# Performance work log

Measured on AMD Instinct MI355X. Metric: run time of the kernel, lower is better.

## Reference

```python
import jax, jax.numpy as jnp
import numpy as np

N_NODES = 100000
N_EDGES = 600000
D_IN = 128
D_OUT = 128


def setup_inputs() -> dict:
    key = jax.random.key(0)
    ks = jax.random.split(key, 8)
    stdv = 1.0 / np.sqrt(D_OUT)
    return {
        "x": jax.random.normal(ks[0], (N_NODES, D_IN), dtype=jnp.float32),
        "edge_src": jax.random.randint(ks[1], (N_EDGES,), 0, N_NODES, dtype=jnp.int32),
        "edge_dst": jax.random.randint(ks[2], (N_EDGES,), 0, N_NODES, dtype=jnp.int32),
        "edge_weight": jax.random.uniform(ks[3], (N_EDGES,), dtype=jnp.float32),
        "weight_l": jax.random.uniform(ks[4], (D_IN, D_OUT), minval=-stdv, maxval=stdv, dtype=jnp.float32),
        "bias_l": jax.random.uniform(ks[5], (D_OUT,), minval=-stdv, maxval=stdv, dtype=jnp.float32),
        "weight_r": jax.random.uniform(ks[6], (D_IN, D_OUT), minval=-stdv, maxval=stdv, dtype=jnp.float32),
        "bias_r": jax.random.uniform(ks[7], (D_OUT,), minval=-stdv, maxval=stdv, dtype=jnp.float32),
    }


def reference(x, edge_src, edge_dst, edge_weight, weight_l, bias_l, weight_r, bias_r):
    # h = input @ weight_l  -> [N, D_OUT]
    h = x @ weight_l
    # spmm(adj, h): out[dst] += adj[dst, src] * h[src]
    msgs = h[edge_src] * edge_weight[:, None]          # [E, D_OUT] gather
    agg = jax.ops.segment_sum(msgs, edge_dst, num_segments=N_NODES)
    out = agg + bias_l
    # root_weight branch (size is None)
    out = out + x @ weight_r + bias_r
    return out
```

## Files before the change

### kernel.cpp

```cpp
#include <hip/hip_runtime.h>
#include <hip/hip_bf16.h>

#define D 128
#define SCAN_BLK 256
#define SCAN_VPT 4
#define SCAN_TILE (SCAN_BLK * SCAN_VPT)

typedef __attribute__((ext_vector_type(8))) short short8;
typedef __attribute__((ext_vector_type(4))) float f32x4;

__global__ __launch_bounds__(256) void prep_w(
    const float* __restrict__ Wl, const float* __restrict__ Wr,
    const float* __restrict__ bl, const float* __restrict__ br,
    __hip_bfloat16* __restrict__ WTl, __hip_bfloat16* __restrict__ WTr,
    float* __restrict__ bsum) {
  const int tid = blockIdx.x * 256 + threadIdx.x;
  const int n = (tid >> 7) & 127;
  const int k = tid & 127;
  if (tid < 16384) {
    WTl[n * D + k] = __float2bfloat16(Wl[k * D + n]);
  } else {
    WTr[n * D + k] = __float2bfloat16(Wr[k * D + n]);
  }
  if (tid < 128) bsum[tid] = bl[tid] + br[tid];
}

__global__ __launch_bounds__(256) void gemm_h(
    const float* __restrict__ x, const __hip_bfloat16* __restrict__ WTl,
    __hip_bfloat16* __restrict__ h,
    const int* __restrict__ edst, int* __restrict__ deg, int n_edges,
    int n_rowtiles) {
  const int gsz = gridDim.x * 256;
  for (int e = blockIdx.x * 256 + threadIdx.x; e < n_edges; e += gsz)
    atomicAdd(&deg[edst[e]], 1);

  __shared__ __hip_bfloat16 xs[16][136];
  const int t = threadIdx.x;
  const int wave = t >> 6;
  const int lane = t & 63;
  const int m = lane & 15;
  const int q = lane >> 4;

  short8 bfrag[2][4];
#pragma unroll
  for (int c = 0; c < 2; ++c) {
    const int n0 = wave * 32 + c * 16;
#pragma unroll
    for (int ks = 0; ks < 4; ++ks)
      bfrag[c][ks] = *(const short8*)&WTl[(n0 + m) * D + ks * 32 + q * 8];
  }

  const int srow = t >> 4;
  const int scol = (t & 15) * 8;

  for (int rt = blockIdx.x; rt < n_rowtiles; rt += gridDim.x) {
    const int rowbase = rt * 16;
    {
      const float4* src = (const float4*)&x[(size_t)(rowbase + srow) * D + scol];
      const float4 v0 = src[0], v1 = src[1];
      __hip_bfloat16* dst = &xs[srow][scol];
      dst[0] = __float2bfloat16(v0.x); dst[1] = __float2bfloat16(v0.y);
      dst[2] = __float2bfloat16(v0.z); dst[3] = __float2bfloat16(v0.w);
      dst[4] = __float2bfloat16(v1.x); dst[5] = __float2bfloat16(v1.y);
      dst[6] = __float2bfloat16(v1.z); dst[7] = __float2bfloat16(v1.w);
    }
    __syncthreads();

    f32x4 acc[2];
#pragma unroll
    for (int c = 0; c < 2; ++c)
#pragma unroll
      for (int r = 0; r < 4; ++r) acc[c][r] = 0.f;

#pragma unroll
    for (int ks = 0; ks < 4; ++ks) {
      const short8 afrag = *(const short8*)&xs[m][ks * 32 + q * 8];
#pragma unroll
      for (int c = 0; c < 2; ++c)
        acc[c] = __builtin_amdgcn_mfma_f32_16x16x32_bf16(afrag, bfrag[c][ks], acc[c], 0, 0, 0);
    }

#pragma unroll
    for (int c = 0; c < 2; ++c) {
      const int n = wave * 32 + c * 16 + m;
#pragma unroll
      for (int r = 0; r < 4; ++r)
        h[(size_t)(rowbase + q * 4 + r) * D + n] = __float2bfloat16(acc[c][r]);
    }
    __syncthreads();
  }
}

__global__ __launch_bounds__(SCAN_BLK) void scan1_kernel(
    const int* __restrict__ deg, int* __restrict__ offsets,
    int* __restrict__ partials, int n) {
  __shared__ int sdata[SCAN_BLK];
  const int t = threadIdx.x;
  const int base = blockIdx.x * SCAN_TILE + t * SCAN_VPT;

  int v[SCAN_VPT];
  int s = 0;
#pragma unroll
  for (int j = 0; j < SCAN_VPT; ++j) {
    v[j] = (base + j < n) ? deg[base + j] : 0;
    s += v[j];
  }
  sdata[t] = s;
  __syncthreads();
  for (int off = 1; off < SCAN_BLK; off <<= 1) {
    int xv = (t >= off) ? sdata[t - off] : 0;
    __syncthreads();
    sdata[t] += xv;
    __syncthreads();
  }
  int excl = sdata[t] - s;
  if (t == SCAN_BLK - 1) partials[blockIdx.x] = sdata[t];
  int run = excl;
#pragma unroll
  for (int j = 0; j < SCAN_VPT; ++j) {
    if (base + j < n) offsets[base + j] = run;
    run += v[j];
  }
}

__global__ __launch_bounds__(SCAN_BLK) void scan3_kernel(
    int* __restrict__ offsets, int* __restrict__ pos,
    const int* __restrict__ partials, int n, int n_edges) {
  __shared__ int s_add;
  const int t = threadIdx.x;
  if (t < 64) {
    int v = 0;
    for (int j = t; j < blockIdx.x; j += 64) v += partials[j];
#pragma unroll
    for (int off = 32; off > 0; off >>= 1) v += __shfl_down(v, off);
    if (t == 0) s_add = v;
  }
  __syncthreads();
  const int add = s_add;
  const int base = blockIdx.x * SCAN_TILE + t * SCAN_VPT;
#pragma unroll
  for (int j = 0; j < SCAN_VPT; ++j) {
    const int i = base + j;
    if (i < n) {
      const int o = offsets[i] + add;
      offsets[i] = o;
      pos[i] = o;
    }
  }
  if (blockIdx.x == 0 && t == 0) offsets[n] = n_edges;
}

__global__ __launch_bounds__(256) void scatter_kernel(
    const int* __restrict__ esrc, const int* __restrict__ edst,
    const float* __restrict__ ew, int* __restrict__ pos,
    int2* __restrict__ pairs, int n_edges) {
  const int e = blockIdx.x * 256 + threadIdx.x;
  if (e >= n_edges) return;
  const int d = edst[e];
  const int slot = atomicAdd(&pos[d], 1);
  pairs[slot] = make_int2(esrc[e], __float_as_int(ew[e]));
}

__global__ __launch_bounds__(256) void sage_out(
    const float* __restrict__ x, const __hip_bfloat16* __restrict__ WTr,
    const float* __restrict__ bsum, const __hip_bfloat16* __restrict__ h,
    const int* __restrict__ offsets, const int2* __restrict__ pairs,
    float* __restrict__ out) {
  __shared__ __hip_bfloat16 xs[16][136];
  __shared__ float ot[16][D];
  const int t = threadIdx.x;
  const int wave = t >> 6;
  const int lane = t & 63;
  const int m = lane & 15;
  const int q = lane >> 4;
  const int rowbase = blockIdx.x * 16;

  short8 bfrag[2][4];
#pragma unroll
  for (int c = 0; c < 2; ++c) {
    const int n0 = wave * 32 + c * 16;
#pragma unroll
    for (int ks = 0; ks < 4; ++ks)
      bfrag[c][ks] = *(const short8*)&WTr[(n0 + m) * D + ks * 32 + q * 8];
  }

  {
    const int srow = t >> 4;
    const int scol = (t & 15) * 8;
    const float4* src = (const float4*)&x[(size_t)(rowbase + srow) * D + scol];
    const float4 v0 = src[0], v1 = src[1];
    __hip_bfloat16* dst = &xs[srow][scol];
    dst[0] = __float2bfloat16(v0.x); dst[1] = __float2bfloat16(v0.y);
    dst[2] = __float2bfloat16(v0.z); dst[3] = __float2bfloat16(v0.w);
    dst[4] = __float2bfloat16(v1.x); dst[5] = __float2bfloat16(v1.y);
    dst[6] = __float2bfloat16(v1.z); dst[7] = __float2bfloat16(v1.w);
  }
  __syncthreads();

  f32x4 acc[2];
#pragma unroll
  for (int c = 0; c < 2; ++c)
#pragma unroll
    for (int r = 0; r < 4; ++r) acc[c][r] = 0.f;

#pragma unroll
  for (int ks = 0; ks < 4; ++ks) {
    const short8 afrag = *(const short8*)&xs[m][ks * 32 + q * 8];
#pragma unroll
    for (int c = 0; c < 2; ++c)
      acc[c] = __builtin_amdgcn_mfma_f32_16x16x32_bf16(afrag, bfrag[c][ks], acc[c], 0, 0, 0);
  }

#pragma unroll
  for (int c = 0; c < 2; ++c) {
    const int n = wave * 32 + c * 16 + m;
    const float b = bsum[n];
#pragma unroll
    for (int r = 0; r < 4; ++r)
      ot[q * 4 + r][n] = acc[c][r] + b;
  }
  __syncthreads();

  const __hip_bfloat162* __restrict__ h2 = (const __hip_bfloat162*)h;
#pragma unroll
  for (int j = 0; j < 4; ++j) {
    const int ln = wave * 4 + j;
    const int node = rowbase + ln;
    const int begin = offsets[node];
    const int end = offsets[node + 1];

    float2 a = *(const float2*)&ot[ln][2 * lane];

    int i = begin;
    for (; i + 4 <= end; i += 4) {
      const int2 p0 = pairs[i + 0];
      const int2 p1 = pairs[i + 1];
      const int2 p2 = pairs[i + 2];
      const int2 p3 = pairs[i + 3];
      const __hip_bfloat162 a0 = h2[(size_t)p0.x * (D / 2) + lane];
      const __hip_bfloat162 a1 = h2[(size_t)p1.x * (D / 2) + lane];
      const __hip_bfloat162 a2 = h2[(size_t)p2.x * (D / 2) + lane];
      const __hip_bfloat162 a3 = h2[(size_t)p3.x * (D / 2) + lane];
      const float w0 = __int_as_float(p0.y), w1 = __int_as_float(p1.y);
      const float w2 = __int_as_float(p2.y), w3 = __int_as_float(p3.y);
      a.x = fmaf(w0, __bfloat162float(a0.x), a.x);
      a.y = fmaf(w0, __bfloat162float(a0.y), a.y);
      a.x = fmaf(w1, __bfloat162float(a1.x), a.x);
      a.y = fmaf(w1, __bfloat162float(a1.y), a.y);
      a.x = fmaf(w2, __bfloat162float(a2.x), a.x);
      a.y = fmaf(w2, __bfloat162float(a2.y), a.y);
      a.x = fmaf(w3, __bfloat162float(a3.x), a.x);
      a.y = fmaf(w3, __bfloat162float(a3.y), a.y);
    }
    for (; i < end; ++i) {
      const int2 p = pairs[i];
      const __hip_bfloat162 av = h2[(size_t)p.x * (D / 2) + lane];
      const float w = __int_as_float(p.y);
      a.x = fmaf(w, __bfloat162float(av.x), a.x);
      a.y = fmaf(w, __bfloat162float(av.y), a.y);
    }
    *(float2*)&out[(size_t)node * D + 2 * lane] = a;
  }
}

extern "C" void kernel_launch(void* const* d_in, const int* in_sizes, int n_in,
                              void* d_out, int out_size, void* d_ws, size_t ws_size,
                              hipStream_t stream) {
  const float* x   = (const float*)d_in[0];
  const int* esrc  = (const int*)d_in[1];
  const int* edst  = (const int*)d_in[2];
  const float* ew  = (const float*)d_in[3];
  const float* Wl  = (const float*)d_in[4];
  const float* bl  = (const float*)d_in[5];
  const float* Wr  = (const float*)d_in[6];
  const float* br  = (const float*)d_in[7];
  float* out = (float*)d_out;

  const int n_nodes = in_sizes[0] / D;
  const int n_edges = in_sizes[1];

  char* ws = (char*)d_ws;
  size_t off = 0;
  __hip_bfloat16* h = (__hip_bfloat16*)(ws + off);
  off += (size_t)n_nodes * D * sizeof(__hip_bfloat16);
  off = (off + 15) & ~15ull;
  int* offsets = (int*)(ws + off);
  off += (size_t)(n_nodes + 1) * sizeof(int);
  off = (off + 15) & ~15ull;
  int* pos = (int*)(ws + off);
  off += (size_t)n_nodes * sizeof(int);
  off = (off + 15) & ~15ull;
  int* partials = (int*)(ws + off);
  off += 1024 * sizeof(int);
  off = (off + 15) & ~15ull;
  int2* pairs = (int2*)(ws + off);
  off += (size_t)n_edges * sizeof(int2);
  off = (off + 15) & ~15ull;
  __hip_bfloat16* WTl = (__hip_bfloat16*)(ws + off);
  off += (size_t)D * D * sizeof(__hip_bfloat16);
  __hip_bfloat16* WTr = (__hip_bfloat16*)(ws + off);
  off += (size_t)D * D * sizeof(__hip_bfloat16);
  float* bsum = (float*)(ws + off);
  off += D * sizeof(float);

  const int n_rowtiles = (n_nodes + 15) / 16;

  hipMemsetAsync(pos, 0, (size_t)n_nodes * sizeof(int), stream);
  prep_w<<<128, 256, 0, stream>>>(Wl, Wr, bl, br, WTl, WTr, bsum);

  const int gemm_grid = n_rowtiles < 2048 ? n_rowtiles : 2048;
  gemm_h<<<gemm_grid, 256, 0, stream>>>(x, WTl, h, edst, pos, n_edges, n_rowtiles);

  const int nparts = (n_nodes + SCAN_TILE - 1) / SCAN_TILE;
  scan1_kernel<<<nparts, SCAN_BLK, 0, stream>>>(pos, offsets, partials, n_nodes);
  scan3_kernel<<<nparts, SCAN_BLK, 0, stream>>>(offsets, pos, partials, n_nodes, n_edges);
  scatter_kernel<<<(n_edges + 255) / 256, 256, 0, stream>>>(esrc, edst, ew, pos, pairs, n_edges);

  sage_out<<<n_rowtiles, 256, 0, stream>>>(x, WTr, bsum, h, offsets, pairs, out);
}
```

Measured before the change: 236.8 us.

## Fuse memset into prep kernel and replace two-pass scan with decoupled lookback

Folds the pos memset and scan-state reset into the weight-prep kernel, and merges the two scan kernels into a single decoupled-lookback scan that chains block prefixes through flag-tagged state words. It also overlaps the xs and ot shared buffers in sage_out, padding ot rows to 130 floats, which needs an extra barrier. The goal is fewer launches and less launch overhead. The scan reads deg from pos and writes offsets back into pos in the same kernel; each thread reads only its own entries before writing them, so this is safe, but the lookback spin relies on earlier blocks being scheduled first.

```diff
diff --git a/kernel.cpp b/kernel.cpp
--- a/kernel.cpp
+++ b/kernel.cpp
@@ -9,20 +9,22 @@
 typedef __attribute__((ext_vector_type(8))) short short8;
 typedef __attribute__((ext_vector_type(4))) float f32x4;
 
-__global__ __launch_bounds__(256) void prep_w(
+__global__ __launch_bounds__(256) void prep_zero(
     const float* __restrict__ Wl, const float* __restrict__ Wr,
     const float* __restrict__ bl, const float* __restrict__ br,
     __hip_bfloat16* __restrict__ WTl, __hip_bfloat16* __restrict__ WTr,
-    float* __restrict__ bsum) {
-  const int tid = blockIdx.x * 256 + threadIdx.x;
-  const int n = (tid >> 7) & 127;
-  const int k = tid & 127;
-  if (tid < 16384) {
+    float* __restrict__ bsum, int* __restrict__ pos,
+    unsigned long long* __restrict__ scan_state, int n_nodes) {
+  const int gtid = blockIdx.x * 256 + threadIdx.x;
+  const int gsz = gridDim.x * 256;
+  for (int i = gtid; i < D * D; i += gsz) {
+    const int n = i >> 7, k = i & 127;
     WTl[n * D + k] = __float2bfloat16(Wl[k * D + n]);
-  } else {
     WTr[n * D + k] = __float2bfloat16(Wr[k * D + n]);
   }
-  if (tid < 128) bsum[tid] = bl[tid] + br[tid];
+  if (gtid < D) bsum[gtid] = bl[gtid] + br[gtid];
+  for (int i = gtid; i < n_nodes; i += gsz) pos[i] = 0;
+  if (gtid < 128) scan_state[gtid] = 0ull;
 }
 
 __global__ __launch_bounds__(256) void gemm_h(
@@ -65,13 +67,11 @@
       dst[6] = __float2bfloat16(v1.z); dst[7] = __float2bfloat16(v1.w);
     }
     __syncthreads();
-
     f32x4 acc[2];
 #pragma unroll
     for (int c = 0; c < 2; ++c)
 #pragma unroll
       for (int r = 0; r < 4; ++r) acc[c][r] = 0.f;
-
 #pragma unroll
     for (int ks = 0; ks < 4; ++ks) {
       const short8 afrag = *(const short8*)&xs[m][ks * 32 + q * 8];
@@ -79,7 +79,6 @@
       for (int c = 0; c < 2; ++c)
         acc[c] = __builtin_amdgcn_mfma_f32_16x16x32_bf16(afrag, bfrag[c][ks], acc[c], 0, 0, 0);
     }
-
 #pragma unroll
     for (int c = 0; c < 2; ++c) {
       const int n = wave * 32 + c * 16 + m;
@@ -91,12 +90,15 @@
   }
 }
 
-__global__ __launch_bounds__(SCAN_BLK) void scan1_kernel(
+__global__ __launch_bounds__(SCAN_BLK) void scan_lb(
     const int* __restrict__ deg, int* __restrict__ offsets,
-    int* __restrict__ partials, int n) {
+    int* __restrict__ pos, unsigned long long* __restrict__ state,
+    int n, int n_edges) {
   __shared__ int sdata[SCAN_BLK];
+  __shared__ int s_base;
   const int t = threadIdx.x;
-  const int base = blockIdx.x * SCAN_TILE + t * SCAN_VPT;
+  const int b = blockIdx.x;
+  const int base = b * SCAN_TILE + t * SCAN_VPT;
 
   int v[SCAN_VPT];
   int s = 0;
@@ -113,41 +115,46 @@
     sdata[t] += xv;
     __syncthreads();
   }
-  int excl = sdata[t] - s;
-  if (t == SCAN_BLK - 1) partials[blockIdx.x] = sdata[t];
-  int run = excl;
-#pragma unroll
-  for (int j = 0; j < SCAN_VPT; ++j) {
-    if (base + j < n) offsets[base + j] = run;
-    run += v[j];
-  }
-}
-
-__global__ __launch_bounds__(SCAN_BLK) void scan3_kernel(
-    int* __restrict__ offsets, int* __restrict__ pos,
-    const int* __restrict__ partials, int n, int n_edges) {
-  __shared__ int s_add;
-  const int t = threadIdx.x;
-  if (t < 64) {
-    int v = 0;
-    for (int j = t; j < blockIdx.x; j += 64) v += partials[j];
-#pragma unroll
-    for (int off = 32; off > 0; off >>= 1) v += __shfl_down(v, off);
-    if (t == 0) s_add = v;
-  }
-  __syncthreads();
-  const int add = s_add;
-  const int base = blockIdx.x * SCAN_TILE + t * SCAN_VPT;
+  const int excl = sdata[t] - s;
+  const int total = sdata[SCAN_BLK - 1];
+
+  if (t == 0) {
+    if (b == 0) {
+      __hip_atomic_store(&state[0], (2ull << 32) | (unsigned)total,
+                         __ATOMIC_RELEASE, __HIP_MEMORY_SCOPE_AGENT);
+      s_base = 0;
+    } else {
+      __hip_atomic_store(&state[b], (1ull << 32) | (unsigned)total,
+                         __ATOMIC_RELEASE, __HIP_MEMORY_SCOPE_AGENT);
+      int run = 0;
+      int j = b - 1;
+      while (true) {
+        const unsigned long long st = __hip_atomic_load(
+            &state[j], __ATOMIC_ACQUIRE, __HIP_MEMORY_SCOPE_AGENT);
+        const unsigned flag = (unsigned)(st >> 32);
+        if (flag == 0) { __builtin_amdgcn_s_sleep(1); continue; }
+        run += (int)(unsigned)st;
+        if (flag == 2) break;
+        --j;
+      }
+      __hip_atomic_store(&state[b], (2ull << 32) | (unsigned)(run + total),
+                         __ATOMIC_RELEASE, __HIP_MEMORY_SCOPE_AGENT);
+      s_base = run;
+    }
+  }
+  __syncthreads();
+
+  int run2 = s_base + excl;
 #pragma unroll
   for (int j = 0; j < SCAN_VPT; ++j) {
     const int i = base + j;
     if (i < n) {
-      const int o = offsets[i] + add;
-      offsets[i] = o;
-      pos[i] = o;
-    }
-  }
-  if (blockIdx.x == 0 && t == 0) offsets[n] = n_edges;
+      offsets[i] = run2;
+      pos[i] = run2;
+      run2 += v[j];
+    }
+  }
+  if (b == 0 && t == 0) offsets[n] = n_edges;
 }
 
 __global__ __launch_bounds__(256) void scatter_kernel(
@@ -166,8 +173,10 @@
     const float* __restrict__ bsum, const __hip_bfloat16* __restrict__ h,
     const int* __restrict__ offsets, const int2* __restrict__ pairs,
     float* __restrict__ out) {
-  __shared__ __hip_bfloat16 xs[16][136];
-  __shared__ float ot[16][D];
+  __shared__ __align__(16) char smraw[16 * 130 * 4];
+  __hip_bfloat16 (*xs)[136] = (__hip_bfloat16(*)[136])smraw;
+  float (*ot)[130] = (float(*)[130])smraw;
+
   const int t = threadIdx.x;
   const int wave = t >> 6;
   const int lane = t & 63;
@@ -202,7 +211,6 @@
   for (int c = 0; c < 2; ++c)
 #pragma unroll
     for (int r = 0; r < 4; ++r) acc[c][r] = 0.f;
-
 #pragma unroll
   for (int ks = 0; ks < 4; ++ks) {
     const short8 afrag = *(const short8*)&xs[m][ks * 32 + q * 8];
@@ -210,6 +218,7 @@
     for (int c = 0; c < 2; ++c)
       acc[c] = __builtin_amdgcn_mfma_f32_16x16x32_bf16(afrag, bfrag[c][ks], acc[c], 0, 0, 0);
   }
+  __syncthreads();
 
 #pragma unroll
   for (int c = 0; c < 2; ++c) {
@@ -228,9 +237,7 @@
     const int node = rowbase + ln;
     const int begin = offsets[node];
     const int end = offsets[node + 1];
-
     float2 a = *(const float2*)&ot[ln][2 * lane];
-
     int i = begin;
     for (; i + 4 <= end; i += 4) {
       const int2 p0 = pairs[i + 0];
@@ -290,9 +297,8 @@
   int* pos = (int*)(ws + off);
   off += (size_t)n_nodes * sizeof(int);
   off = (off + 15) & ~15ull;
-  int* partials = (int*)(ws + off);
-  off += 1024 * sizeof(int);
-  off = (off + 15) & ~15ull;
+  unsigned long long* scan_state = (unsigned long long*)(ws + off);
+  off += 128 * sizeof(unsigned long long);
   int2* pairs = (int2*)(ws + off);
   off += (size_t)n_edges * sizeof(int2);
   off = (off + 15) & ~15ull;
@@ -305,15 +311,16 @@
 
   const int n_rowtiles = (n_nodes + 15) / 16;
 
-  hipMemsetAsync(pos, 0, (size_t)n_nodes * sizeof(int), stream);
-  prep_w<<<128, 256, 0, stream>>>(Wl, Wr, bl, br, WTl, WTr, bsum);
+  prep_zero<<<256, 256, 0, stream>>>(Wl, Wr, bl, br, WTl, WTr, bsum, pos,
+                                     scan_state, n_nodes);
 
   const int gemm_grid = n_rowtiles < 2048 ? n_rowtiles : 2048;
   gemm_h<<<gemm_grid, 256, 0, stream>>>(x, WTl, h, edst, pos, n_edges, n_rowtiles);
 
   const int nparts = (n_nodes + SCAN_TILE - 1) / SCAN_TILE;
-  scan1_kernel<<<nparts, SCAN_BLK, 0, stream>>>(pos, offsets, partials, n_nodes);
-  scan3_kernel<<<nparts, SCAN_BLK, 0, stream>>>(offsets, pos, partials, n_nodes, n_edges);
+  scan_lb<<<nparts, SCAN_BLK, 0, stream>>>(pos, offsets, pos, scan_state,
+                                           n_nodes, n_edges);
+
   scatter_kernel<<<(n_edges + 255) / 256, 256, 0, stream>>>(esrc, edst, ew, pos, pairs, n_edges);
 
   sage_out<<<n_rowtiles, 256, 0, stream>>>(x, WTr, bsum, h, offsets, pairs, out);
```

After: 248.3 us. 1.05x slower.

## Aggregate raw features before projection and fuse both GEMMs into one kernel

Applied to the files above, without the earlier changes.

Uses associativity to reorder the SAGE layer: raw fp32 x rows are gathered and summed per destination first, and (A·x)·Wl is computed afterwards instead of A·(x·Wl). This removes the separate h GEMM kernel. Both projections now run in one MFMA kernel that reads the bf16 aggregate and x together. The edge-degree histogram moves into the weight-prep kernel. In exchange the gather reads fp32 x rows (twice the bytes of the old bf16 h), and the aggregate is rounded to bf16 before the GEMM.

```diff
diff --git a/kernel.cpp b/kernel.cpp
--- a/kernel.cpp
+++ b/kernel.cpp
@@ -9,86 +9,21 @@
 typedef __attribute__((ext_vector_type(8))) short short8;
 typedef __attribute__((ext_vector_type(4))) float f32x4;
 
-__global__ __launch_bounds__(256) void prep_w(
+__global__ __launch_bounds__(256) void prep_hist(
     const float* __restrict__ Wl, const float* __restrict__ Wr,
     const float* __restrict__ bl, const float* __restrict__ br,
     __hip_bfloat16* __restrict__ WTl, __hip_bfloat16* __restrict__ WTr,
-    float* __restrict__ bsum) {
-  const int tid = blockIdx.x * 256 + threadIdx.x;
-  const int n = (tid >> 7) & 127;
-  const int k = tid & 127;
-  if (tid < 16384) {
+    float* __restrict__ bsum, int* __restrict__ pos,
+    const int* __restrict__ edst, int n_edges) {
+  const int gtid = blockIdx.x * 256 + threadIdx.x;
+  const int gsz = gridDim.x * 256;
+  for (int i = gtid; i < D * D; i += gsz) {
+    const int k = i >> 7, n = i & 127;
     WTl[n * D + k] = __float2bfloat16(Wl[k * D + n]);
-  } else {
     WTr[n * D + k] = __float2bfloat16(Wr[k * D + n]);
   }
-  if (tid < 128) bsum[tid] = bl[tid] + br[tid];
-}
-
-__global__ __launch_bounds__(256) void gemm_h(
-    const float* __restrict__ x, const __hip_bfloat16* __restrict__ WTl,
-    __hip_bfloat16* __restrict__ h,
-    const int* __restrict__ edst, int* __restrict__ deg, int n_edges,
-    int n_rowtiles) {
-  const int gsz = gridDim.x * 256;
-  for (int e = blockIdx.x * 256 + threadIdx.x; e < n_edges; e += gsz)
-    atomicAdd(&deg[edst[e]], 1);
-
-  __shared__ __hip_bfloat16 xs[16][136];
-  const int t = threadIdx.x;
-  const int wave = t >> 6;
-  const int lane = t & 63;
-  const int m = lane & 15;
-  const int q = lane >> 4;
-
-  short8 bfrag[2][4];
-#pragma unroll
-  for (int c = 0; c < 2; ++c) {
-    const int n0 = wave * 32 + c * 16;
-#pragma unroll
-    for (int ks = 0; ks < 4; ++ks)
-      bfrag[c][ks] = *(const short8*)&WTl[(n0 + m) * D + ks * 32 + q * 8];
-  }
-
-  const int srow = t >> 4;
-  const int scol = (t & 15) * 8;
-
-  for (int rt = blockIdx.x; rt < n_rowtiles; rt += gridDim.x) {
-    const int rowbase = rt * 16;
-    {
-      const float4* src = (const float4*)&x[(size_t)(rowbase + srow) * D + scol];
-      const float4 v0 = src[0], v1 = src[1];
-      __hip_bfloat16* dst = &xs[srow][scol];
-      dst[0] = __float2bfloat16(v0.x); dst[1] = __float2bfloat16(v0.y);
-      dst[2] = __float2bfloat16(v0.z); dst[3] = __float2bfloat16(v0.w);
-      dst[4] = __float2bfloat16(v1.x); dst[5] = __float2bfloat16(v1.y);
-      dst[6] = __float2bfloat16(v1.z); dst[7] = __float2bfloat16(v1.w);
-    }
-    __syncthreads();
-
-    f32x4 acc[2];
-#pragma unroll
-    for (int c = 0; c < 2; ++c)
-#pragma unroll
-      for (int r = 0; r < 4; ++r) acc[c][r] = 0.f;
-
-#pragma unroll
-    for (int ks = 0; ks < 4; ++ks) {
-      const short8 afrag = *(const short8*)&xs[m][ks * 32 + q * 8];
-#pragma unroll
-      for (int c = 0; c < 2; ++c)
-        acc[c] = __builtin_amdgcn_mfma_f32_16x16x32_bf16(afrag, bfrag[c][ks], acc[c], 0, 0, 0);
-    }
-
-#pragma unroll
-    for (int c = 0; c < 2; ++c) {
-      const int n = wave * 32 + c * 16 + m;
-#pragma unroll
-      for (int r = 0; r < 4; ++r)
-        h[(size_t)(rowbase + q * 4 + r) * D + n] = __float2bfloat16(acc[c][r]);
-    }
-    __syncthreads();
-  }
+  if (gtid < D) bsum[gtid] = bl[gtid] + br[gtid];
+  for (int e = gtid; e < n_edges; e += gsz) atomicAdd(&pos[edst[e]], 1);
 }
 
 __global__ __launch_bounds__(SCAN_BLK) void scan1_kernel(
@@ -130,7 +65,7 @@
   const int t = threadIdx.x;
   if (t < 64) {
     int v = 0;
-    for (int j = t; j < blockIdx.x; j += 64) v += partials[j];
+    for (int j = t; j < (int)blockIdx.x; j += 64) v += partials[j];
 #pragma unroll
     for (int off = 32; off > 0; off >>= 1) v += __shfl_down(v, off);
     if (t == 0) s_add = v;
@@ -161,13 +96,52 @@
   pairs[slot] = make_int2(esrc[e], __float_as_int(ew[e]));
 }
 
-__global__ __launch_bounds__(256) void sage_out(
-    const float* __restrict__ x, const __hip_bfloat16* __restrict__ WTr,
-    const float* __restrict__ bsum, const __hip_bfloat16* __restrict__ h,
-    const int* __restrict__ offsets, const int2* __restrict__ pairs,
-    float* __restrict__ out) {
+__global__ __launch_bounds__(256) void spmm(
+    const float* __restrict__ x, const int* __restrict__ offsets,
+    const int2* __restrict__ pairs, __hip_bfloat16* __restrict__ agg,
+    int n_nodes) {
+  const int node = blockIdx.x * 4 + (threadIdx.x >> 6);
+  if (node >= n_nodes) return;
+  const int t = threadIdx.x & 63;
+  const int begin = offsets[node];
+  const int end = offsets[node + 1];
+
+  float2 a = make_float2(0.f, 0.f);
+  int i = begin;
+  for (; i + 4 <= end; i += 4) {
+    const int2 p0 = pairs[i + 0];
+    const int2 p1 = pairs[i + 1];
+    const int2 p2 = pairs[i + 2];
+    const int2 p3 = pairs[i + 3];
+    const float2 v0 = *(const float2*)&x[(size_t)p0.x * D + 2 * t];
+    const float2 v1 = *(const float2*)&x[(size_t)p1.x * D + 2 * t];
+    const float2 v2 = *(const float2*)&x[(size_t)p2.x * D + 2 * t];
+    const float2 v3 = *(const float2*)&x[(size_t)p3.x * D + 2 * t];
+    const float w0 = __int_as_float(p0.y), w1 = __int_as_float(p1.y);
+    const float w2 = __int_as_float(p2.y), w3 = __int_as_float(p3.y);
+    a.x = fmaf(w0, v0.x, a.x); a.y = fmaf(w0, v0.y, a.y);
+    a.x = fmaf(w1, v1.x, a.x); a.y = fmaf(w1, v1.y, a.y);
+    a.x = fmaf(w2, v2.x, a.x); a.y = fmaf(w2, v2.y, a.y);
+    a.x = fmaf(w3, v3.x, a.x); a.y = fmaf(w3, v3.y, a.y);
+  }
+  for (; i < end; ++i) {
+    const int2 p = pairs[i];
+    const float2 v = *(const float2*)&x[(size_t)p.x * D + 2 * t];
+    const float w = __int_as_float(p.y);
+    a.x = fmaf(w, v.x, a.x); a.y = fmaf(w, v.y, a.y);
+  }
+  __hip_bfloat162 o;
+  o.x = __float2bfloat16(a.x);
+  o.y = __float2bfloat16(a.y);
+  *(__hip_bfloat162*)&agg[(size_t)node * D + 2 * t] = o;
+}
+
+__global__ __launch_bounds__(256) void gemm_out(
+    const float* __restrict__ x, const __hip_bfloat16* __restrict__ agg,
+    const __hip_bfloat16* __restrict__ WTl, const __hip_bfloat16* __restrict__ WTr,
+    const float* __restrict__ bsum, float* __restrict__ out) {
   __shared__ __hip_bfloat16 xs[16][136];
-  __shared__ float ot[16][D];
+  __shared__ __hip_bfloat16 as[16][136];
   const int t = threadIdx.x;
   const int wave = t >> 6;
   const int lane = t & 63;
@@ -175,13 +149,15 @@
   const int q = lane >> 4;
   const int rowbase = blockIdx.x * 16;
 
-  short8 bfrag[2][4];
+  short8 bx[2][4], ba[2][4];
 #pragma unroll
   for (int c = 0; c < 2; ++c) {
     const int n0 = wave * 32 + c * 16;
 #pragma unroll
-    for (int ks = 0; ks < 4; ++ks)
-      bfrag[c][ks] = *(const short8*)&WTr[(n0 + m) * D + ks * 32 + q * 8];
+    for (int ks = 0; ks < 4; ++ks) {
+      bx[c][ks] = *(const short8*)&WTr[(n0 + m) * D + ks * 32 + q * 8];
+      ba[c][ks] = *(const short8*)&WTl[(n0 + m) * D + ks * 32 + q * 8];
+    }
   }
 
   {
@@ -194,6 +170,7 @@
     dst[2] = __float2bfloat16(v0.z); dst[3] = __float2bfloat16(v0.w);
     dst[4] = __float2bfloat16(v1.x); dst[5] = __float2bfloat16(v1.y);
     dst[6] = __float2bfloat16(v1.z); dst[7] = __float2bfloat16(v1.w);
+    *(float4*)&as[srow][scol] = *(const float4*)&agg[(size_t)(rowbase + srow) * D + scol];
   }
   __syncthreads();
 
@@ -205,10 +182,13 @@
 
 #pragma unroll
   for (int ks = 0; ks < 4; ++ks) {
-    const short8 afrag = *(const short8*)&xs[m][ks * 32 + q * 8];
-#pragma unroll
-    for (int c = 0; c < 2; ++c)
-      acc[c] = __builtin_amdgcn_mfma_f32_16x16x32_bf16(afrag, bfrag[c][ks], acc[c], 0, 0, 0);
+    const short8 afx = *(const short8*)&xs[m][ks * 32 + q * 8];
+    const short8 afa = *(const short8*)&as[m][ks * 32 + q * 8];
+#pragma unroll
+    for (int c = 0; c < 2; ++c) {
+      acc[c] = __builtin_amdgcn_mfma_f32_16x16x32_bf16(afx, bx[c][ks], acc[c], 0, 0, 0);
+      acc[c] = __builtin_amdgcn_mfma_f32_16x16x32_bf16(afa, ba[c][ks], acc[c], 0, 0, 0);
+    }
   }
 
 #pragma unroll
@@ -217,49 +197,7 @@
     const float b = bsum[n];
 #pragma unroll
     for (int r = 0; r < 4; ++r)
-      ot[q * 4 + r][n] = acc[c][r] + b;
-  }
-  __syncthreads();
-
-  const __hip_bfloat162* __restrict__ h2 = (const __hip_bfloat162*)h;
-#pragma unroll
-  for (int j = 0; j < 4; ++j) {
-    const int ln = wave * 4 + j;
-    const int node = rowbase + ln;
-    const int begin = offsets[node];
-    const int end = offsets[node + 1];
-
-    float2 a = *(const float2*)&ot[ln][2 * lane];
-
-    int i = begin;
-    for (; i + 4 <= end; i += 4) {
-      const int2 p0 = pairs[i + 0];
-      const int2 p1 = pairs[i + 1];
-      const int2 p2 = pairs[i + 2];
-      const int2 p3 = pairs[i + 3];
-      const __hip_bfloat162 a0 = h2[(size_t)p0.x * (D / 2) + lane];
-      const __hip_bfloat162 a1 = h2[(size_t)p1.x * (D / 2) + lane];
-      const __hip_bfloat162 a2 = h2[(size_t)p2.x * (D / 2) + lane];
-      const __hip_bfloat162 a3 = h2[(size_t)p3.x * (D / 2) + lane];
-      const float w0 = __int_as_float(p0.y), w1 = __int_as_float(p1.y);
-      const float w2 = __int_as_float(p2.y), w3 = __int_as_float(p3.y);
-      a.x = fmaf(w0, __bfloat162float(a0.x), a.x);
-      a.y = fmaf(w0, __bfloat162float(a0.y), a.y);
-      a.x = fmaf(w1, __bfloat162float(a1.x), a.x);
-      a.y = fmaf(w1, __bfloat162float(a1.y), a.y);
-      a.x = fmaf(w2, __bfloat162float(a2.x), a.x);
-      a.y = fmaf(w2, __bfloat162float(a2.y), a.y);
-      a.x = fmaf(w3, __bfloat162float(a3.x), a.x);
-      a.y = fmaf(w3, __bfloat162float(a3.y), a.y);
-    }
-    for (; i < end; ++i) {
-      const int2 p = pairs[i];
-      const __hip_bfloat162 av = h2[(size_t)p.x * (D / 2) + lane];
-      const float w = __int_as_float(p.y);
-      a.x = fmaf(w, __bfloat162float(av.x), a.x);
-      a.y = fmaf(w, __bfloat162float(av.y), a.y);
-    }
-    *(float2*)&out[(size_t)node * D + 2 * lane] = a;
+      out[(size_t)(rowbase + q * 4 + r) * D + n] = acc[c][r] + b;
   }
 }
 
@@ -281,7 +219,7 @@
 
   char* ws = (char*)d_ws;
   size_t off = 0;
-  __hip_bfloat16* h = (__hip_bfloat16*)(ws + off);
+  __hip_bfloat16* agg = (__hip_bfloat16*)(ws + off);
   off += (size_t)n_nodes * D * sizeof(__hip_bfloat16);
   off = (off + 15) & ~15ull;
   int* offsets = (int*)(ws + off);
@@ -306,15 +244,17 @@
   const int n_rowtiles = (n_nodes + 15) / 16;
 
   hipMemsetAsync(pos, 0, (size_t)n_nodes * sizeof(int), stream);
-  prep_w<<<128, 256, 0, stream>>>(Wl, Wr, bl, br, WTl, WTr, bsum);
-
-  const int gemm_grid = n_rowtiles < 2048 ? n_rowtiles : 2048;
-  gemm_h<<<gemm_grid, 256, 0, stream>>>(x, WTl, h, edst, pos, n_edges, n_rowtiles);
+
+  prep_hist<<<1024, 256, 0, stream>>>(Wl, Wr, bl, br, WTl, WTr, bsum, pos,
+                                      edst, n_edges);
 
   const int nparts = (n_nodes + SCAN_TILE - 1) / SCAN_TILE;
   scan1_kernel<<<nparts, SCAN_BLK, 0, stream>>>(pos, offsets, partials, n_nodes);
   scan3_kernel<<<nparts, SCAN_BLK, 0, stream>>>(offsets, pos, partials, n_nodes, n_edges);
+
   scatter_kernel<<<(n_edges + 255) / 256, 256, 0, stream>>>(esrc, edst, ew, pos, pairs, n_edges);
 
-  sage_out<<<n_rowtiles, 256, 0, stream>>>(x, WTr, bsum, h, offsets, pairs, out);
-}
+  spmm<<<(n_nodes + 3) / 4, 256, 0, stream>>>(x, offsets, pairs, agg, n_nodes);
+
+  gemm_out<<<n_rowtiles, 256, 0, stream>>>(x, agg, WTl, WTr, bsum, out);
+}
```

Result: slower. 269.6 us (+13.8%).
